# Kernel tuning notes

Hardware: AMD Instinct MI355X
Metric: run time of the kernel (lower is better)

The kernel has to match this reference:

```python
import jax, jax.numpy as jnp
import numpy as np

NEG_SLOPE = 0.2   # PyG GATConv leaky_relu default
BN_EPS = 1e-5


def setup_inputs() -> dict:
    key = jax.random.key(0)
    ks = jax.random.split(key, 6)
    B, C, N, T = 8, 128, 64, 512   # batch, in_channels, electrodes, time_steps
    H, D = 4, 32                   # heads, per-head dim; OUT = H*D = 128
    E = 256                        # knn edges (k=4 per electrode)
    OUT = H * D
    x = jax.random.normal(ks[0], (B, C, N, T), dtype=jnp.float32)
    W = jax.random.normal(ks[1], (C, H, D), dtype=jnp.float32) / np.float32(np.sqrt(C))
    att_src = jax.random.normal(ks[2], (H, D), dtype=jnp.float32) / np.float32(np.sqrt(D))
    att_dst = jax.random.normal(ks[3], (H, D), dtype=jnp.float32) / np.float32(np.sqrt(D))
    bias = jnp.zeros((OUT,), dtype=jnp.float32)
    bn_gamma = jnp.ones((OUT,), jnp.float32)
    bn_beta = jnp.zeros((OUT,), jnp.float32)
    bn_mean = jnp.zeros((OUT,), jnp.float32)   # BatchNorm running stats (eval mode)
    bn_var = jnp.ones((OUT,), jnp.float32)
    edge_index = jax.random.randint(ks[4], (2, E), 0, N, dtype=jnp.int32)
    return dict(x=x, W=W, att_src=att_src, att_dst=att_dst, bias=bias,
                bn_gamma=bn_gamma, bn_beta=bn_beta, bn_mean=bn_mean,
                bn_var=bn_var, edge_index=edge_index)


def _gat(x, W, att_src, att_dst, bias, edge_index):
    # x: [BT, N, C]; fixed graph shared across all BT slices -> fully batched
    BT, N, C = x.shape
    H, D = att_src.shape
    loops = jnp.arange(N, dtype=edge_index.dtype)
    src = jnp.concatenate([edge_index[0], loops])   # GATConv add_self_loops=True
    dst = jnp.concatenate([edge_index[1], loops])   # [E']
    h = jnp.einsum('bnc,chd->bnhd', x, W)           # [BT,N,H,D]
    a_src = jnp.einsum('bnhd,hd->bnh', h, att_src)  # [BT,N,H]
    a_dst = jnp.einsum('bnhd,hd->bnh', h, att_dst)
    scores = jax.nn.leaky_relu(a_src[:, src] + a_dst[:, dst], NEG_SLOPE)  # [BT,E',H]
    scores_e = jnp.transpose(scores, (1, 0, 2))                           # [E',BT,H]
    # segment softmax over incoming edges of each target node
    m = jax.ops.segment_max(scores_e, dst, num_segments=N)               # [N,BT,H]
    ex = jnp.exp(scores_e - m[dst])
    denom = jax.ops.segment_sum(ex, dst, num_segments=N)
    alpha = ex / denom[dst]                                               # [E',BT,H]
    msgs = alpha[..., None] * jnp.transpose(h[:, src], (1, 0, 2, 3))      # [E',BT,H,D]
    agg = jax.ops.segment_sum(msgs, dst, num_segments=N)                  # [N,BT,H,D]
    out = jnp.transpose(agg, (1, 0, 2, 3)).reshape(BT, N, H * D) + bias   # concat heads
    return out


def reference(x, W, att_src, att_dst, bias, bn_gamma, bn_beta, bn_mean, bn_var, edge_index):
    B, C, N, T = x.shape
    xt = jnp.transpose(x, (0, 3, 2, 1)).reshape(B * T, N, C)  # loop dim batched
    g = _gat(xt, W, att_src, att_dst, bias, edge_index)        # [BT,N,OUT]
    g = g.mean(axis=1)                                         # mean over nodes -> [BT,OUT]
    OUT = g.shape[-1]
    g = g.reshape(B, T, OUT).transpose(0, 2, 1)                # [B,OUT,T]
    y = (g - bn_mean[:, None]) * jax.lax.rsqrt(bn_var[:, None] + BN_EPS) \
        * bn_gamma[:, None] + bn_beta[:, None]                 # BatchNorm1d (eval)
    return y[:, :, None, :]                                    # [B,OUT,1,T]
```

## Files before the change

### kernel.cpp

```cpp
#include <hip/hip_runtime.h>
#include <math.h>

#define B_ 8
#define C_ 128
#define N_ 64
#define T_ 512
#define H_ 4
#define D_ 32
#define OUT_ 128
#define E_ 256
#define EP_ 320
#define NEG_SLOPE 0.2f
#define BN_EPS 1e-5f
#define TC 16

__global__ void setup_kernel(const float* __restrict__ W,
                             const float* __restrict__ att_src,
                             const float* __restrict__ att_dst,
                             const int* __restrict__ edge_index,
                             float* __restrict__ wa,
                             int* __restrict__ iOff_g, int* __restrict__ iSrc_g,
                             int* __restrict__ oOff_g, int* __restrict__ oDst_g) {
  __shared__ int icnt[N_], ibase[N_ + 1], ifill[N_];
  __shared__ int ocnt[N_], obase[N_ + 1], ofill[N_];
  __shared__ int esrc[EP_], edst[EP_];
  int tid = threadIdx.x;

  for (int idx = tid; idx < C_ * 8; idx += blockDim.x) {
    int c = idx >> 3, j = idx & 7, h = j & 3;
    const float* att = (j < 4) ? att_src : att_dst;
    float s = 0.f;
    for (int d = 0; d < D_; ++d)
      s += W[(c * H_ + h) * D_ + d] * att[h * D_ + d];
    wa[idx] = s;
  }
  if (tid < N_) { icnt[tid] = 0; ifill[tid] = 0; ocnt[tid] = 0; ofill[tid] = 0; }
  __syncthreads();
  for (int e = tid; e < EP_; e += blockDim.x) {
    int s, d;
    if (e < E_) { s = edge_index[e]; d = edge_index[E_ + e]; }
    else        { s = e - E_;        d = e - E_; }
    esrc[e] = s; edst[e] = d;
    atomicAdd(&icnt[d], 1);
    atomicAdd(&ocnt[s], 1);
  }
  __syncthreads();
  if (tid == 0) {
    int ai = 0, ao = 0;
    for (int n = 0; n < N_; ++n) {
      ibase[n] = ai; ai += icnt[n];
      obase[n] = ao; ao += ocnt[n];
    }
    ibase[N_] = ai; obase[N_] = ao;
  }
  __syncthreads();
  if (tid <= N_) { iOff_g[tid] = ibase[tid]; oOff_g[tid] = obase[tid]; }
  for (int e = tid; e < EP_; e += blockDim.x) {
    int s = esrc[e], d = edst[e];
    int pi = ibase[d] + atomicAdd(&ifill[d], 1);
    iSrc_g[pi] = s;
    int po = obase[s] + atomicAdd(&ofill[s], 1);
    oDst_g[po] = d;
  }
}

__global__ __launch_bounds__(256, 1)
void mega_kernel(const float* __restrict__ x,
                 const float* __restrict__ wa_g,
                 const float* __restrict__ W,
                 const int* __restrict__ iOff_g, const int* __restrict__ iSrc_g,
                 const int* __restrict__ oOff_g, const int* __restrict__ oDst_g,
                 const float* __restrict__ bias,
                 const float* __restrict__ bn_gamma,
                 const float* __restrict__ bn_beta,
                 const float* __restrict__ bn_mean,
                 const float* __restrict__ bn_var,
                 float* __restrict__ out) {
  __shared__ float a_l[8 * 64 * 20];
  __shared__ float m_l[64 * 16 * 4];
  __shared__ float inv_l[64 * 16 * 4];
  __shared__ float w_l[64 * 4 * 16];
  __shared__ float wal[C_ * 8];
  __shared__ int iOff[N_ + 1], oOff[N_ + 1];
  __shared__ int iSrc[EP_], oDst[EP_];

  const int tid = threadIdx.x;
  const int xcd = blockIdx.x & 7;
  const int jj  = blockIdx.x >> 3;
  const int pair = xcd * 16 + (jj & 15);
  const int parity = jj >> 4;
  const int b  = pair >> 4;
  const int tc = ((pair & 15) << 1) | parity;
  const int t0 = tc * TC;

  for (int i = tid; i < EP_; i += 256) { iSrc[i] = iSrc_g[i]; oDst[i] = oDst_g[i]; }
  if (tid <= N_) { iOff[tid] = iOff_g[tid]; oOff[tid] = oOff_g[tid]; }
  for (int i = tid; i < C_ * 8; i += 256) wal[i] = wa_g[i];
  __syncthreads();

  {
    const int n1 = tid >> 2, q = tid & 3;
    const float* xp = x + ((size_t)(b * C_) * N_ + n1) * T_ + t0 + q * 4;
    float acc[8][4];
#pragma unroll
    for (int j = 0; j < 8; ++j)
#pragma unroll
      for (int tt = 0; tt < 4; ++tt) acc[j][tt] = 0.f;
#pragma unroll 4
    for (int c = 0; c < C_; ++c) {
      float4 xv = *reinterpret_cast<const float4*>(xp + (size_t)c * (N_ * T_));
      float xq[4] = {xv.x, xv.y, xv.z, xv.w};
#pragma unroll
      for (int j = 0; j < 8; ++j) {
        float wj = wal[c * 8 + j];
#pragma unroll
        for (int tt = 0; tt < 4; ++tt) acc[j][tt] = fmaf(xq[tt], wj, acc[j][tt]);
      }
    }
#pragma unroll
    for (int j = 0; j < 8; ++j) {
      float4 v; v.x = acc[j][0]; v.y = acc[j][1]; v.z = acc[j][2]; v.w = acc[j][3];
      *reinterpret_cast<float4*>(&a_l[j * 1280 + n1 * 20 + q * 4]) = v;
    }
  }
  __syncthreads();

  {
    const int t = tid & 15, grp = tid >> 4;
#pragma unroll
    for (int rep = 0; rep < 4; ++rep) {
      int nd = grp + rep * 16;
      int e0 = iOff[nd], e1 = iOff[nd + 1];
      float ad0 = a_l[4 * 1280 + nd * 20 + t];
      float ad1 = a_l[5 * 1280 + nd * 20 + t];
      float ad2 = a_l[6 * 1280 + nd * 20 + t];
      float ad3 = a_l[7 * 1280 + nd * 20 + t];
      float m0 = -1e30f, m1 = -1e30f, m2 = -1e30f, m3 = -1e30f;
      for (int e = e0; e < e1; ++e) {
        int s = iSrc[e];
        float v0 = a_l[0 * 1280 + s * 20 + t] + ad0; v0 = v0 > 0.f ? v0 : NEG_SLOPE * v0;
        float v1 = a_l[1 * 1280 + s * 20 + t] + ad1; v1 = v1 > 0.f ? v1 : NEG_SLOPE * v1;
        float v2 = a_l[2 * 1280 + s * 20 + t] + ad2; v2 = v2 > 0.f ? v2 : NEG_SLOPE * v2;
        float v3 = a_l[3 * 1280 + s * 20 + t] + ad3; v3 = v3 > 0.f ? v3 : NEG_SLOPE * v3;
        m0 = fmaxf(m0, v0); m1 = fmaxf(m1, v1);
        m2 = fmaxf(m2, v2); m3 = fmaxf(m3, v3);
      }
      float d0 = 0.f, d1 = 0.f, d2 = 0.f, d3 = 0.f;
      for (int e = e0; e < e1; ++e) {
        int s = iSrc[e];
        float v0 = a_l[0 * 1280 + s * 20 + t] + ad0; v0 = v0 > 0.f ? v0 : NEG_SLOPE * v0;
        float v1 = a_l[1 * 1280 + s * 20 + t] + ad1; v1 = v1 > 0.f ? v1 : NEG_SLOPE * v1;
        float v2 = a_l[2 * 1280 + s * 20 + t] + ad2; v2 = v2 > 0.f ? v2 : NEG_SLOPE * v2;
        float v3 = a_l[3 * 1280 + s * 20 + t] + ad3; v3 = v3 > 0.f ? v3 : NEG_SLOPE * v3;
        d0 += __expf(v0 - m0); d1 += __expf(v1 - m1);
        d2 += __expf(v2 - m2); d3 += __expf(v3 - m3);
      }
      float4 mv; mv.x = m0; mv.y = m1; mv.z = m2; mv.w = m3;
      float4 iv; iv.x = 1.f / (d0 * (float)N_); iv.y = 1.f / (d1 * (float)N_);
      iv.z = 1.f / (d2 * (float)N_); iv.w = 1.f / (d3 * (float)N_);
      *reinterpret_cast<float4*>(&m_l[(nd * 16 + t) * 4]) = mv;
      *reinterpret_cast<float4*>(&inv_l[(nd * 16 + t) * 4]) = iv;
    }
  }
  __syncthreads();

  {
    const int t = tid & 15, grp = tid >> 4;
#pragma unroll
    for (int rep = 0; rep < 4; ++rep) {
      int src = grp + rep * 16;
      int e0 = oOff[src], e1 = oOff[src + 1];
      float as0 = a_l[0 * 1280 + src * 20 + t];
      float as1 = a_l[1 * 1280 + src * 20 + t];
      float as2 = a_l[2 * 1280 + src * 20 + t];
      float as3 = a_l[3 * 1280 + src * 20 + t];
      float w0 = 0.f, w1 = 0.f, w2 = 0.f, w3 = 0.f;
      for (int e = e0; e < e1; ++e) {
        int d = oDst[e];
        float4 mv = *reinterpret_cast<const float4*>(&m_l[(d * 16 + t) * 4]);
        float4 iv = *reinterpret_cast<const float4*>(&inv_l[(d * 16 + t) * 4]);
        float v0 = as0 + a_l[4 * 1280 + d * 20 + t]; v0 = v0 > 0.f ? v0 : NEG_SLOPE * v0;
        float v1 = as1 + a_l[5 * 1280 + d * 20 + t]; v1 = v1 > 0.f ? v1 : NEG_SLOPE * v1;
        float v2 = as2 + a_l[6 * 1280 + d * 20 + t]; v2 = v2 > 0.f ? v2 : NEG_SLOPE * v2;
        float v3 = as3 + a_l[7 * 1280 + d * 20 + t]; v3 = v3 > 0.f ? v3 : NEG_SLOPE * v3;
        w0 += __expf(v0 - mv.x) * iv.x;
        w1 += __expf(v1 - mv.y) * iv.y;
        w2 += __expf(v2 - mv.z) * iv.z;
        w3 += __expf(v3 - mv.w) * iv.w;
      }
      w_l[src * 64 +  0 + t] = w0;
      w_l[src * 64 + 16 + t] = w1;
      w_l[src * 64 + 32 + t] = w2;
      w_l[src * 64 + 48 + t] = w3;
    }
  }
  __syncthreads();

  {
    const int t2 = tid & 15, cl = tid >> 4;
    const float* xb = x + ((size_t)(b * C_) + cl) * N_ * T_ + t0 + t2;
    float yr[8][4];
#pragma unroll
    for (int cg = 0; cg < 8; ++cg)
#pragma unroll
      for (int h = 0; h < 4; ++h) yr[cg][h] = 0.f;
#pragma unroll 2
    for (int n = 0; n < N_; ++n) {
      float w0 = w_l[n * 64 +  0 + t2];
      float w1 = w_l[n * 64 + 16 + t2];
      float w2 = w_l[n * 64 + 32 + t2];
      float w3 = w_l[n * 64 + 48 + t2];
#pragma unroll
      for (int cg = 0; cg < 8; ++cg) {
        float xv = xb[(size_t)cg * 16 * N_ * T_ + (size_t)n * T_];
        yr[cg][0] = fmaf(xv, w0, yr[cg][0]);
        yr[cg][1] = fmaf(xv, w1, yr[cg][1]);
        yr[cg][2] = fmaf(xv, w2, yr[cg][2]);
        yr[cg][3] = fmaf(xv, w3, yr[cg][3]);
      }
    }
    float* y_l = a_l;
#pragma unroll
    for (int cg = 0; cg < 8; ++cg)
#pragma unroll
      for (int h = 0; h < 4; ++h)
        y_l[h * 2176 + (cg * 16 + cl) * 17 + t2] = yr[cg][h];
  }
  __syncthreads();

  {
    const int t3 = tid & 15, g = tid >> 4;
    const int h = g >> 2, d0 = (g & 3) * 8;
    const float* y_l = a_l;
    float acc[8];
#pragma unroll
    for (int k = 0; k < 8; ++k) acc[k] = 0.f;
#pragma unroll 4
    for (int c = 0; c < C_; ++c) {
      float yv = y_l[h * 2176 + c * 17 + t3];
      const float4 wv0 = *reinterpret_cast<const float4*>(
          &W[((size_t)c * H_ + h) * D_ + d0]);
      const float4 wv1 = *reinterpret_cast<const float4*>(
          &W[((size_t)c * H_ + h) * D_ + d0 + 4]);
      acc[0] = fmaf(yv, wv0.x, acc[0]); acc[1] = fmaf(yv, wv0.y, acc[1]);
      acc[2] = fmaf(yv, wv0.z, acc[2]); acc[3] = fmaf(yv, wv0.w, acc[3]);
      acc[4] = fmaf(yv, wv1.x, acc[4]); acc[5] = fmaf(yv, wv1.y, acc[5]);
      acc[6] = fmaf(yv, wv1.z, acc[6]); acc[7] = fmaf(yv, wv1.w, acc[7]);
    }
#pragma unroll
    for (int k = 0; k < 8; ++k) {
      int oc = h * D_ + d0 + k;
      float scale = bn_gamma[oc] * rsqrtf(bn_var[oc] + BN_EPS);
      float shift = bn_beta[oc] - bn_mean[oc] * scale;
      out[((size_t)b * OUT_ + oc) * T_ + t0 + t3] =
          (acc[k] + bias[oc]) * scale + shift;
    }
  }
}

extern "C" void kernel_launch(void* const* d_in, const int* in_sizes, int n_in,
                              void* d_out, int out_size, void* d_ws, size_t ws_size,
                              hipStream_t stream) {
  const float* x        = (const float*)d_in[0];
  const float* W        = (const float*)d_in[1];
  const float* att_src  = (const float*)d_in[2];
  const float* att_dst  = (const float*)d_in[3];
  const float* bias     = (const float*)d_in[4];
  const float* bn_gamma = (const float*)d_in[5];
  const float* bn_beta  = (const float*)d_in[6];
  const float* bn_mean  = (const float*)d_in[7];
  const float* bn_var   = (const float*)d_in[8];
  const int* edge_index = (const int*)d_in[9];
  float* out = (float*)d_out;

  char* ws = (char*)d_ws;
  float* wa   = (float*)ws;
  int* iOff_g = (int*)(ws + 4096);
  int* iSrc_g = (int*)(ws + 4608);
  int* oOff_g = (int*)(ws + 6144);
  int* oDst_g = (int*)(ws + 6656);

  setup_kernel<<<1, 256, 0, stream>>>(W, att_src, att_dst, edge_index, wa,
                                      iOff_g, iSrc_g, oOff_g, oDst_g);
  mega_kernel<<<256, 256, 0, stream>>>(x, wa, W, iOff_g, iSrc_g, oOff_g, oDst_g,
                                       bias, bn_gamma, bn_beta, bn_mean, bn_var,
                                       out);
}
```

Baseline: 77.38 us.

## Halve time chunk per block to launch 512 blocks with two blocks per CU

Reduces the per-block time tile from 16 to 8 steps, doubling the grid to 512 blocks and raising launch bounds so two blocks can co-reside per CU. Shared buffers shrink and every phase's thread mapping is redone: x loads become float2/float4 with new strides, the aggregation phase is re-tiled so each thread covers one channel and four time steps, and the XCD-aware block remap is replaced by a plain batch/chunk split. The aim is better occupancy and latency hiding for the memory-bound x reads. In exchange each block reloads the graph tables and weights for half as much work, and losing the XCD mapping may reduce L2 locality.

```diff
diff --git a/kernel.cpp b/kernel.cpp
--- a/kernel.cpp
+++ b/kernel.cpp
@@ -12,7 +12,7 @@
 #define EP_ 320
 #define NEG_SLOPE 0.2f
 #define BN_EPS 1e-5f
-#define TC 16
+#define TC 8
 
 __global__ void setup_kernel(const float* __restrict__ W,
                              const float* __restrict__ att_src,
@@ -64,7 +64,7 @@
   }
 }
 
-__global__ __launch_bounds__(256, 1)
+__global__ __launch_bounds__(256, 2)
 void mega_kernel(const float* __restrict__ x,
                  const float* __restrict__ wa_g,
                  const float* __restrict__ W,
@@ -76,22 +76,18 @@
                  const float* __restrict__ bn_mean,
                  const float* __restrict__ bn_var,
                  float* __restrict__ out) {
-  __shared__ float a_l[8 * 64 * 20];
-  __shared__ float m_l[64 * 16 * 4];
-  __shared__ float inv_l[64 * 16 * 4];
-  __shared__ float w_l[64 * 4 * 16];
+  __shared__ float a_l[8 * 64 * 12];
+  __shared__ float m_l[64 * 9 * 4];
+  __shared__ float inv_l[64 * 9 * 4];
+  __shared__ float w_l[64 * 36];
   __shared__ float wal[C_ * 8];
   __shared__ int iOff[N_ + 1], oOff[N_ + 1];
   __shared__ int iSrc[EP_], oDst[EP_];
 
   const int tid = threadIdx.x;
-  const int xcd = blockIdx.x & 7;
-  const int jj  = blockIdx.x >> 3;
-  const int pair = xcd * 16 + (jj & 15);
-  const int parity = jj >> 4;
-  const int b  = pair >> 4;
-  const int tc = ((pair & 15) << 1) | parity;
-  const int t0 = tc * TC;
+  const int b = blockIdx.x & 7;
+  const int tchunk = blockIdx.x >> 3;
+  const int t0 = tchunk * TC;
 
   for (int i = tid; i < EP_; i += 256) { iSrc[i] = iSrc_g[i]; oDst[i] = oDst_g[i]; }
   if (tid <= N_) { iOff[tid] = iOff_g[tid]; oOff[tid] = oOff_g[tid]; }
@@ -100,155 +96,146 @@
 
   {
     const int n1 = tid >> 2, q = tid & 3;
-    const float* xp = x + ((size_t)(b * C_) * N_ + n1) * T_ + t0 + q * 4;
-    float acc[8][4];
-#pragma unroll
-    for (int j = 0; j < 8; ++j)
-#pragma unroll
-      for (int tt = 0; tt < 4; ++tt) acc[j][tt] = 0.f;
-#pragma unroll 4
+    const float* xp = x + ((size_t)(b * C_) * N_ + n1) * T_ + t0 + q * 2;
+    float acc[8][2];
+#pragma unroll
+    for (int j = 0; j < 8; ++j) { acc[j][0] = 0.f; acc[j][1] = 0.f; }
+#pragma unroll 8
     for (int c = 0; c < C_; ++c) {
-      float4 xv = *reinterpret_cast<const float4*>(xp + (size_t)c * (N_ * T_));
-      float xq[4] = {xv.x, xv.y, xv.z, xv.w};
+      float2 xv = *reinterpret_cast<const float2*>(xp + (size_t)c * (N_ * T_));
 #pragma unroll
       for (int j = 0; j < 8; ++j) {
         float wj = wal[c * 8 + j];
-#pragma unroll
-        for (int tt = 0; tt < 4; ++tt) acc[j][tt] = fmaf(xq[tt], wj, acc[j][tt]);
+        acc[j][0] = fmaf(xv.x, wj, acc[j][0]);
+        acc[j][1] = fmaf(xv.y, wj, acc[j][1]);
       }
     }
 #pragma unroll
     for (int j = 0; j < 8; ++j) {
-      float4 v; v.x = acc[j][0]; v.y = acc[j][1]; v.z = acc[j][2]; v.w = acc[j][3];
-      *reinterpret_cast<float4*>(&a_l[j * 1280 + n1 * 20 + q * 4]) = v;
-    }
-  }
-  __syncthreads();
-
-  {
-    const int t = tid & 15, grp = tid >> 4;
-#pragma unroll
-    for (int rep = 0; rep < 4; ++rep) {
-      int nd = grp + rep * 16;
+      float2 v; v.x = acc[j][0]; v.y = acc[j][1];
+      *reinterpret_cast<float2*>(&a_l[j * 768 + n1 * 12 + q * 2]) = v;
+    }
+  }
+  __syncthreads();
+
+  {
+    const int t = tid & 7, grp = tid >> 3;
+#pragma unroll
+    for (int rep = 0; rep < 2; ++rep) {
+      int nd = grp + rep * 32;
       int e0 = iOff[nd], e1 = iOff[nd + 1];
-      float ad0 = a_l[4 * 1280 + nd * 20 + t];
-      float ad1 = a_l[5 * 1280 + nd * 20 + t];
-      float ad2 = a_l[6 * 1280 + nd * 20 + t];
-      float ad3 = a_l[7 * 1280 + nd * 20 + t];
+      float ad0 = a_l[4 * 768 + nd * 12 + t];
+      float ad1 = a_l[5 * 768 + nd * 12 + t];
+      float ad2 = a_l[6 * 768 + nd * 12 + t];
+      float ad3 = a_l[7 * 768 + nd * 12 + t];
       float m0 = -1e30f, m1 = -1e30f, m2 = -1e30f, m3 = -1e30f;
       for (int e = e0; e < e1; ++e) {
         int s = iSrc[e];
-        float v0 = a_l[0 * 1280 + s * 20 + t] + ad0; v0 = v0 > 0.f ? v0 : NEG_SLOPE * v0;
-        float v1 = a_l[1 * 1280 + s * 20 + t] + ad1; v1 = v1 > 0.f ? v1 : NEG_SLOPE * v1;
-        float v2 = a_l[2 * 1280 + s * 20 + t] + ad2; v2 = v2 > 0.f ? v2 : NEG_SLOPE * v2;
-        float v3 = a_l[3 * 1280 + s * 20 + t] + ad3; v3 = v3 > 0.f ? v3 : NEG_SLOPE * v3;
+        float v0 = a_l[0 * 768 + s * 12 + t] + ad0; v0 = v0 > 0.f ? v0 : NEG_SLOPE * v0;
+        float v1 = a_l[1 * 768 + s * 12 + t] + ad1; v1 = v1 > 0.f ? v1 : NEG_SLOPE * v1;
+        float v2 = a_l[2 * 768 + s * 12 + t] + ad2; v2 = v2 > 0.f ? v2 : NEG_SLOPE * v2;
+        float v3 = a_l[3 * 768 + s * 12 + t] + ad3; v3 = v3 > 0.f ? v3 : NEG_SLOPE * v3;
         m0 = fmaxf(m0, v0); m1 = fmaxf(m1, v1);
         m2 = fmaxf(m2, v2); m3 = fmaxf(m3, v3);
       }
       float d0 = 0.f, d1 = 0.f, d2 = 0.f, d3 = 0.f;
       for (int e = e0; e < e1; ++e) {
         int s = iSrc[e];
-        float v0 = a_l[0 * 1280 + s * 20 + t] + ad0; v0 = v0 > 0.f ? v0 : NEG_SLOPE * v0;
-        float v1 = a_l[1 * 1280 + s * 20 + t] + ad1; v1 = v1 > 0.f ? v1 : NEG_SLOPE * v1;
-        float v2 = a_l[2 * 1280 + s * 20 + t] + ad2; v2 = v2 > 0.f ? v2 : NEG_SLOPE * v2;
-        float v3 = a_l[3 * 1280 + s * 20 + t] + ad3; v3 = v3 > 0.f ? v3 : NEG_SLOPE * v3;
+        float v0 = a_l[0 * 768 + s * 12 + t] + ad0; v0 = v0 > 0.f ? v0 : NEG_SLOPE * v0;
+        float v1 = a_l[1 * 768 + s * 12 + t] + ad1; v1 = v1 > 0.f ? v1 : NEG_SLOPE * v1;
+        float v2 = a_l[2 * 768 + s * 12 + t] + ad2; v2 = v2 > 0.f ? v2 : NEG_SLOPE * v2;
+        float v3 = a_l[3 * 768 + s * 12 + t] + ad3; v3 = v3 > 0.f ? v3 : NEG_SLOPE * v3;
         d0 += __expf(v0 - m0); d1 += __expf(v1 - m1);
         d2 += __expf(v2 - m2); d3 += __expf(v3 - m3);
       }
       float4 mv; mv.x = m0; mv.y = m1; mv.z = m2; mv.w = m3;
       float4 iv; iv.x = 1.f / (d0 * (float)N_); iv.y = 1.f / (d1 * (float)N_);
       iv.z = 1.f / (d2 * (float)N_); iv.w = 1.f / (d3 * (float)N_);
-      *reinterpret_cast<float4*>(&m_l[(nd * 16 + t) * 4]) = mv;
-      *reinterpret_cast<float4*>(&inv_l[(nd * 16 + t) * 4]) = iv;
-    }
-  }
-  __syncthreads();
-
-  {
-    const int t = tid & 15, grp = tid >> 4;
-#pragma unroll
-    for (int rep = 0; rep < 4; ++rep) {
-      int src = grp + rep * 16;
+      *reinterpret_cast<float4*>(&m_l[(nd * 9 + t) * 4]) = mv;
+      *reinterpret_cast<float4*>(&inv_l[(nd * 9 + t) * 4]) = iv;
+    }
+  }
+  __syncthreads();
+
+  {
+    const int t = tid & 7, grp = tid >> 3;
+#pragma unroll
+    for (int rep = 0; rep < 2; ++rep) {
+      int src = grp + rep * 32;
       int e0 = oOff[src], e1 = oOff[src + 1];
-      float as0 = a_l[0 * 1280 + src * 20 + t];
-      float as1 = a_l[1 * 1280 + src * 20 + t];
-      float as2 = a_l[2 * 1280 + src * 20 + t];
-      float as3 = a_l[3 * 1280 + src * 20 + t];
+      float as0 = a_l[0 * 768 + src * 12 + t];
+      float as1 = a_l[1 * 768 + src * 12 + t];
+      float as2 = a_l[2 * 768 + src * 12 + t];
+      float as3 = a_l[3 * 768 + src * 12 + t];
       float w0 = 0.f, w1 = 0.f, w2 = 0.f, w3 = 0.f;
       for (int e = e0; e < e1; ++e) {
         int d = oDst[e];
-        float4 mv = *reinterpret_cast<const float4*>(&m_l[(d * 16 + t) * 4]);
-        float4 iv = *reinterpret_cast<const float4*>(&inv_l[(d * 16 + t) * 4]);
-        float v0 = as0 + a_l[4 * 1280 + d * 20 + t]; v0 = v0 > 0.f ? v0 : NEG_SLOPE * v0;
-        float v1 = as1 + a_l[5 * 1280 + d * 20 + t]; v1 = v1 > 0.f ? v1 : NEG_SLOPE * v1;
-        float v2 = as2 + a_l[6 * 1280 + d * 20 + t]; v2 = v2 > 0.f ? v2 : NEG_SLOPE * v2;
-        float v3 = as3 + a_l[7 * 1280 + d * 20 + t]; v3 = v3 > 0.f ? v3 : NEG_SLOPE * v3;
+        float4 mv = *reinterpret_cast<const float4*>(&m_l[(d * 9 + t) * 4]);
+        float4 iv = *reinterpret_cast<const float4*>(&inv_l[(d * 9 + t) * 4]);
+        float v0 = as0 + a_l[4 * 768 + d * 12 + t]; v0 = v0 > 0.f ? v0 : NEG_SLOPE * v0;
+        float v1 = as1 + a_l[5 * 768 + d * 12 + t]; v1 = v1 > 0.f ? v1 : NEG_SLOPE * v1;
+        float v2 = as2 + a_l[6 * 768 + d * 12 + t]; v2 = v2 > 0.f ? v2 : NEG_SLOPE * v2;
+        float v3 = as3 + a_l[7 * 768 + d * 12 + t]; v3 = v3 > 0.f ? v3 : NEG_SLOPE * v3;
         w0 += __expf(v0 - mv.x) * iv.x;
         w1 += __expf(v1 - mv.y) * iv.y;
         w2 += __expf(v2 - mv.z) * iv.z;
         w3 += __expf(v3 - mv.w) * iv.w;
       }
-      w_l[src * 64 +  0 + t] = w0;
-      w_l[src * 64 + 16 + t] = w1;
-      w_l[src * 64 + 32 + t] = w2;
-      w_l[src * 64 + 48 + t] = w3;
-    }
-  }
-  __syncthreads();
-
-  {
-    const int t2 = tid & 15, cl = tid >> 4;
-    const float* xb = x + ((size_t)(b * C_) + cl) * N_ * T_ + t0 + t2;
-    float yr[8][4];
-#pragma unroll
-    for (int cg = 0; cg < 8; ++cg)
-#pragma unroll
-      for (int h = 0; h < 4; ++h) yr[cg][h] = 0.f;
-#pragma unroll 2
+      w_l[src * 36 +  0 + t] = w0;
+      w_l[src * 36 +  8 + t] = w1;
+      w_l[src * 36 + 16 + t] = w2;
+      w_l[src * 36 + 24 + t] = w3;
+    }
+  }
+  __syncthreads();
+
+  {
+    const int cl = tid >> 1, g = tid & 1;
+    const float* xb = x + ((size_t)(b * C_) + cl) * N_ * T_ + t0 + g * 4;
+    float yr[4][4];
+#pragma unroll
+    for (int h = 0; h < 4; ++h)
+#pragma unroll
+      for (int tt = 0; tt < 4; ++tt) yr[h][tt] = 0.f;
+#pragma unroll 8
     for (int n = 0; n < N_; ++n) {
-      float w0 = w_l[n * 64 +  0 + t2];
-      float w1 = w_l[n * 64 + 16 + t2];
-      float w2 = w_l[n * 64 + 32 + t2];
-      float w3 = w_l[n * 64 + 48 + t2];
-#pragma unroll
-      for (int cg = 0; cg < 8; ++cg) {
-        float xv = xb[(size_t)cg * 16 * N_ * T_ + (size_t)n * T_];
-        yr[cg][0] = fmaf(xv, w0, yr[cg][0]);
-        yr[cg][1] = fmaf(xv, w1, yr[cg][1]);
-        yr[cg][2] = fmaf(xv, w2, yr[cg][2]);
-        yr[cg][3] = fmaf(xv, w3, yr[cg][3]);
+      float4 xv = *reinterpret_cast<const float4*>(xb + (size_t)n * T_);
+#pragma unroll
+      for (int h = 0; h < 4; ++h) {
+        float4 wv = *reinterpret_cast<const float4*>(&w_l[n * 36 + h * 8 + g * 4]);
+        yr[h][0] = fmaf(xv.x, wv.x, yr[h][0]);
+        yr[h][1] = fmaf(xv.y, wv.y, yr[h][1]);
+        yr[h][2] = fmaf(xv.z, wv.z, yr[h][2]);
+        yr[h][3] = fmaf(xv.w, wv.w, yr[h][3]);
       }
     }
     float* y_l = a_l;
 #pragma unroll
-    for (int cg = 0; cg < 8; ++cg)
-#pragma unroll
-      for (int h = 0; h < 4; ++h)
-        y_l[h * 2176 + (cg * 16 + cl) * 17 + t2] = yr[cg][h];
-  }
-  __syncthreads();
-
-  {
-    const int t3 = tid & 15, g = tid >> 4;
-    const int h = g >> 2, d0 = (g & 3) * 8;
+    for (int h = 0; h < 4; ++h) {
+      float4 v; v.x = yr[h][0]; v.y = yr[h][1]; v.z = yr[h][2]; v.w = yr[h][3];
+      y_l[h * 1152 + cl * 9 + g * 4 + 0] = v.x;
+      y_l[h * 1152 + cl * 9 + g * 4 + 1] = v.y;
+      y_l[h * 1152 + cl * 9 + g * 4 + 2] = v.z;
+      y_l[h * 1152 + cl * 9 + g * 4 + 3] = v.w;
+    }
+  }
+  __syncthreads();
+
+  {
+    const int t3 = tid & 7, g3 = tid >> 3;
+    const int h = g3 >> 3, d0 = (g3 & 7) * 4;
     const float* y_l = a_l;
-    float acc[8];
-#pragma unroll
-    for (int k = 0; k < 8; ++k) acc[k] = 0.f;
+    float acc[4] = {0.f, 0.f, 0.f, 0.f};
 #pragma unroll 4
     for (int c = 0; c < C_; ++c) {
-      float yv = y_l[h * 2176 + c * 17 + t3];
-      const float4 wv0 = *reinterpret_cast<const float4*>(
+      float yv = y_l[h * 1152 + c * 9 + t3];
+      const float4 wv = *reinterpret_cast<const float4*>(
           &W[((size_t)c * H_ + h) * D_ + d0]);
-      const float4 wv1 = *reinterpret_cast<const float4*>(
-          &W[((size_t)c * H_ + h) * D_ + d0 + 4]);
-      acc[0] = fmaf(yv, wv0.x, acc[0]); acc[1] = fmaf(yv, wv0.y, acc[1]);
-      acc[2] = fmaf(yv, wv0.z, acc[2]); acc[3] = fmaf(yv, wv0.w, acc[3]);
-      acc[4] = fmaf(yv, wv1.x, acc[4]); acc[5] = fmaf(yv, wv1.y, acc[5]);
-      acc[6] = fmaf(yv, wv1.z, acc[6]); acc[7] = fmaf(yv, wv1.w, acc[7]);
-    }
-#pragma unroll
-    for (int k = 0; k < 8; ++k) {
+      acc[0] = fmaf(yv, wv.x, acc[0]); acc[1] = fmaf(yv, wv.y, acc[1]);
+      acc[2] = fmaf(yv, wv.z, acc[2]); acc[3] = fmaf(yv, wv.w, acc[3]);
+    }
+#pragma unroll
+    for (int k = 0; k < 4; ++k) {
       int oc = h * D_ + d0 + k;
       float scale = bn_gamma[oc] * rsqrtf(bn_var[oc] + BN_EPS);
       float shift = bn_beta[oc] - bn_mean[oc] * scale;
@@ -282,7 +269,7 @@
 
   setup_kernel<<<1, 256, 0, stream>>>(W, att_src, att_dst, edge_index, wa,
                                       iOff_g, iSrc_g, oOff_g, oDst_g);
-  mega_kernel<<<256, 256, 0, stream>>>(x, wa, W, iOff_g, iSrc_g, oOff_g, oDst_g,
+  mega_kernel<<<512, 256, 0, stream>>>(x, wa, W, iOff_g, iSrc_g, oOff_g, oDst_g,
                                        bias, bn_gamma, bn_beta, bn_mean, bn_var,
                                        out);
 }
```

After: 81.77 us. 5.7% more time.

## Quadruple threads per block with split-K attention projection and LDS-staged W

Applied to the files above, without the earlier changes.

Blocks grow from 256 to 1024 threads. The attention-logit projection is split across four channel quarters and combined through a shared-memory tree reduction. Each thread now handles one node in the softmax stages and half as many channels in the aggregation. The softmax max/inverse is folded into a single scale exp(-m)/denom, and W is staged into LDS for the final projection. The goal is more memory-level parallelism and latency hiding for the x reads. The cost is extra barriers, reduction traffic and a large 112KB shared arena.

```diff
diff --git a/kernel.cpp b/kernel.cpp
--- a/kernel.cpp
+++ b/kernel.cpp
@@ -13,6 +13,7 @@
 #define NEG_SLOPE 0.2f
 #define BN_EPS 1e-5f
 #define TC 16
+#define NT_ (N_ * T_)
 
 __global__ void setup_kernel(const float* __restrict__ W,
                              const float* __restrict__ att_src,
@@ -64,10 +65,10 @@
   }
 }
 
-__global__ __launch_bounds__(256, 1)
+__global__ __launch_bounds__(1024, 1)
 void mega_kernel(const float* __restrict__ x,
                  const float* __restrict__ wa_g,
-                 const float* __restrict__ W,
+                 const float* __restrict__ Wm,
                  const int* __restrict__ iOff_g, const int* __restrict__ iSrc_g,
                  const int* __restrict__ oOff_g, const int* __restrict__ oDst_g,
                  const float* __restrict__ bias,
@@ -76,185 +77,233 @@
                  const float* __restrict__ bn_mean,
                  const float* __restrict__ bn_var,
                  float* __restrict__ out) {
-  __shared__ float a_l[8 * 64 * 20];
-  __shared__ float m_l[64 * 16 * 4];
-  __shared__ float inv_l[64 * 16 * 4];
-  __shared__ float w_l[64 * 4 * 16];
-  __shared__ float wal[C_ * 8];
-  __shared__ int iOff[N_ + 1], oOff[N_ + 1];
-  __shared__ int iSrc[EP_], oDst[EP_];
+  __shared__ __align__(16) char arena[114688];
+  float* a_l   = (float*)arena;
+  float4* redA = (float4*)(arena + 40960);
+  float4* redB = (float4*)(arena + 73728);
+  float* z_l   = (float*)(arena + 40960);
+  float* w_l   = (float*)(arena + 57344);
+  float* wstage= (float*)(arena + 40960);
+  float* wal   = (float*)(arena + 106496);
+  int* iSrc = (int*)(arena + 110592);
+  int* oDst = iSrc + EP_;
+  int* iOff = oDst + EP_;
+  int* oOff = iOff + (N_ + 1);
 
   const int tid = threadIdx.x;
-  const int xcd = blockIdx.x & 7;
-  const int jj  = blockIdx.x >> 3;
-  const int pair = xcd * 16 + (jj & 15);
-  const int parity = jj >> 4;
-  const int b  = pair >> 4;
-  const int tc = ((pair & 15) << 1) | parity;
-  const int t0 = tc * TC;
-
-  for (int i = tid; i < EP_; i += 256) { iSrc[i] = iSrc_g[i]; oDst[i] = oDst_g[i]; }
-  if (tid <= N_) { iOff[tid] = iOff_g[tid]; oOff[tid] = oOff_g[tid]; }
-  for (int i = tid; i < C_ * 8; i += 256) wal[i] = wa_g[i];
-  __syncthreads();
-
-  {
-    const int n1 = tid >> 2, q = tid & 3;
-    const float* xp = x + ((size_t)(b * C_) * N_ + n1) * T_ + t0 + q * 4;
-    float acc[8][4];
-#pragma unroll
-    for (int j = 0; j < 8; ++j)
-#pragma unroll
-      for (int tt = 0; tt < 4; ++tt) acc[j][tt] = 0.f;
-#pragma unroll 4
-    for (int c = 0; c < C_; ++c) {
-      float4 xv = *reinterpret_cast<const float4*>(xp + (size_t)c * (N_ * T_));
-      float xq[4] = {xv.x, xv.y, xv.z, xv.w};
+  const int b = blockIdx.x & 7;
+  const int tchunk = blockIdx.x >> 3;
+  const int t0 = tchunk * TC;
+
+  if (tid < EP_) { iSrc[tid] = iSrc_g[tid]; oDst[tid] = oDst_g[tid]; }
+  if (tid >= EP_ && tid < EP_ + N_ + 1) {
+    int i = tid - EP_;
+    iOff[i] = iOff_g[i]; oOff[i] = oOff_g[i];
+  }
+  if (tid < C_ * 8) wal[tid] = wa_g[tid];
+  __syncthreads();
+
+  {
+    const int q  = tid & 3;
+    const int cq = (tid >> 2) & 3;
+    const int n1 = tid >> 4;
+    const float* xp = x + ((size_t)(b * C_ + cq * 32) * N_ + n1) * T_ + t0 + q * 4;
+    float4 acc[8];
+#pragma unroll
+    for (int j = 0; j < 8; ++j) { acc[j].x = 0.f; acc[j].y = 0.f; acc[j].z = 0.f; acc[j].w = 0.f; }
+    for (int kb = 0; kb < 4; ++kb) {
+      float4 xv[8];
+#pragma unroll
+      for (int u = 0; u < 8; ++u)
+        xv[u] = *reinterpret_cast<const float4*>(xp + (size_t)(kb * 8 + u) * NT_);
+#pragma unroll
+      for (int u = 0; u < 8; ++u) {
+        const int c = cq * 32 + kb * 8 + u;
+        const float4 w0 = *reinterpret_cast<const float4*>(&wal[c * 8]);
+        const float4 w1 = *reinterpret_cast<const float4*>(&wal[c * 8 + 4]);
+        const float4 xu = xv[u];
+        acc[0].x = fmaf(xu.x, w0.x, acc[0].x); acc[0].y = fmaf(xu.y, w0.x, acc[0].y);
+        acc[0].z = fmaf(xu.z, w0.x, acc[0].z); acc[0].w = fmaf(xu.w, w0.x, acc[0].w);
+        acc[1].x = fmaf(xu.x, w0.y, acc[1].x); acc[1].y = fmaf(xu.y, w0.y, acc[1].y);
+        acc[1].z = fmaf(xu.z, w0.y, acc[1].z); acc[1].w = fmaf(xu.w, w0.y, acc[1].w);
+        acc[2].x = fmaf(xu.x, w0.z, acc[2].x); acc[2].y = fmaf(xu.y, w0.z, acc[2].y);
+        acc[2].z = fmaf(xu.z, w0.z, acc[2].z); acc[2].w = fmaf(xu.w, w0.z, acc[2].w);
+        acc[3].x = fmaf(xu.x, w0.w, acc[3].x); acc[3].y = fmaf(xu.y, w0.w, acc[3].y);
+        acc[3].z = fmaf(xu.z, w0.w, acc[3].z); acc[3].w = fmaf(xu.w, w0.w, acc[3].w);
+        acc[4].x = fmaf(xu.x, w1.x, acc[4].x); acc[4].y = fmaf(xu.y, w1.x, acc[4].y);
+        acc[4].z = fmaf(xu.z, w1.x, acc[4].z); acc[4].w = fmaf(xu.w, w1.x, acc[4].w);
+        acc[5].x = fmaf(xu.x, w1.y, acc[5].x); acc[5].y = fmaf(xu.y, w1.y, acc[5].y);
+        acc[5].z = fmaf(xu.z, w1.y, acc[5].z); acc[5].w = fmaf(xu.w, w1.y, acc[5].w);
+        acc[6].x = fmaf(xu.x, w1.z, acc[6].x); acc[6].y = fmaf(xu.y, w1.z, acc[6].y);
+        acc[6].z = fmaf(xu.z, w1.z, acc[6].z); acc[6].w = fmaf(xu.w, w1.z, acc[6].w);
+        acc[7].x = fmaf(xu.x, w1.w, acc[7].x); acc[7].y = fmaf(xu.y, w1.w, acc[7].y);
+        acc[7].z = fmaf(xu.z, w1.w, acc[7].z); acc[7].w = fmaf(xu.w, w1.w, acc[7].w);
+      }
+    }
+    if (cq == 1) {
+#pragma unroll
+      for (int j = 0; j < 8; ++j) redA[(j * 64 + n1) * 4 + q] = acc[j];
+    } else if (cq == 3) {
+#pragma unroll
+      for (int j = 0; j < 8; ++j) redB[(j * 64 + n1) * 4 + q] = acc[j];
+    }
+    __syncthreads();
+    if (cq == 0) {
 #pragma unroll
       for (int j = 0; j < 8; ++j) {
-        float wj = wal[c * 8 + j];
-#pragma unroll
-        for (int tt = 0; tt < 4; ++tt) acc[j][tt] = fmaf(xq[tt], wj, acc[j][tt]);
-      }
-    }
-#pragma unroll
-    for (int j = 0; j < 8; ++j) {
-      float4 v; v.x = acc[j][0]; v.y = acc[j][1]; v.z = acc[j][2]; v.w = acc[j][3];
-      *reinterpret_cast<float4*>(&a_l[j * 1280 + n1 * 20 + q * 4]) = v;
-    }
-  }
-  __syncthreads();
-
-  {
-    const int t = tid & 15, grp = tid >> 4;
-#pragma unroll
-    for (int rep = 0; rep < 4; ++rep) {
-      int nd = grp + rep * 16;
-      int e0 = iOff[nd], e1 = iOff[nd + 1];
-      float ad0 = a_l[4 * 1280 + nd * 20 + t];
-      float ad1 = a_l[5 * 1280 + nd * 20 + t];
-      float ad2 = a_l[6 * 1280 + nd * 20 + t];
-      float ad3 = a_l[7 * 1280 + nd * 20 + t];
-      float m0 = -1e30f, m1 = -1e30f, m2 = -1e30f, m3 = -1e30f;
-      for (int e = e0; e < e1; ++e) {
-        int s = iSrc[e];
-        float v0 = a_l[0 * 1280 + s * 20 + t] + ad0; v0 = v0 > 0.f ? v0 : NEG_SLOPE * v0;
-        float v1 = a_l[1 * 1280 + s * 20 + t] + ad1; v1 = v1 > 0.f ? v1 : NEG_SLOPE * v1;
-        float v2 = a_l[2 * 1280 + s * 20 + t] + ad2; v2 = v2 > 0.f ? v2 : NEG_SLOPE * v2;
-        float v3 = a_l[3 * 1280 + s * 20 + t] + ad3; v3 = v3 > 0.f ? v3 : NEG_SLOPE * v3;
-        m0 = fmaxf(m0, v0); m1 = fmaxf(m1, v1);
-        m2 = fmaxf(m2, v2); m3 = fmaxf(m3, v3);
-      }
-      float d0 = 0.f, d1 = 0.f, d2 = 0.f, d3 = 0.f;
-      for (int e = e0; e < e1; ++e) {
-        int s = iSrc[e];
-        float v0 = a_l[0 * 1280 + s * 20 + t] + ad0; v0 = v0 > 0.f ? v0 : NEG_SLOPE * v0;
-        float v1 = a_l[1 * 1280 + s * 20 + t] + ad1; v1 = v1 > 0.f ? v1 : NEG_SLOPE * v1;
-        float v2 = a_l[2 * 1280 + s * 20 + t] + ad2; v2 = v2 > 0.f ? v2 : NEG_SLOPE * v2;
-        float v3 = a_l[3 * 1280 + s * 20 + t] + ad3; v3 = v3 > 0.f ? v3 : NEG_SLOPE * v3;
-        d0 += __expf(v0 - m0); d1 += __expf(v1 - m1);
-        d2 += __expf(v2 - m2); d3 += __expf(v3 - m3);
-      }
-      float4 mv; mv.x = m0; mv.y = m1; mv.z = m2; mv.w = m3;
-      float4 iv; iv.x = 1.f / (d0 * (float)N_); iv.y = 1.f / (d1 * (float)N_);
-      iv.z = 1.f / (d2 * (float)N_); iv.w = 1.f / (d3 * (float)N_);
-      *reinterpret_cast<float4*>(&m_l[(nd * 16 + t) * 4]) = mv;
-      *reinterpret_cast<float4*>(&inv_l[(nd * 16 + t) * 4]) = iv;
-    }
-  }
-  __syncthreads();
-
-  {
-    const int t = tid & 15, grp = tid >> 4;
-#pragma unroll
-    for (int rep = 0; rep < 4; ++rep) {
-      int src = grp + rep * 16;
-      int e0 = oOff[src], e1 = oOff[src + 1];
-      float as0 = a_l[0 * 1280 + src * 20 + t];
-      float as1 = a_l[1 * 1280 + src * 20 + t];
-      float as2 = a_l[2 * 1280 + src * 20 + t];
-      float as3 = a_l[3 * 1280 + src * 20 + t];
-      float w0 = 0.f, w1 = 0.f, w2 = 0.f, w3 = 0.f;
-      for (int e = e0; e < e1; ++e) {
-        int d = oDst[e];
-        float4 mv = *reinterpret_cast<const float4*>(&m_l[(d * 16 + t) * 4]);
-        float4 iv = *reinterpret_cast<const float4*>(&inv_l[(d * 16 + t) * 4]);
-        float v0 = as0 + a_l[4 * 1280 + d * 20 + t]; v0 = v0 > 0.f ? v0 : NEG_SLOPE * v0;
-        float v1 = as1 + a_l[5 * 1280 + d * 20 + t]; v1 = v1 > 0.f ? v1 : NEG_SLOPE * v1;
-        float v2 = as2 + a_l[6 * 1280 + d * 20 + t]; v2 = v2 > 0.f ? v2 : NEG_SLOPE * v2;
-        float v3 = as3 + a_l[7 * 1280 + d * 20 + t]; v3 = v3 > 0.f ? v3 : NEG_SLOPE * v3;
-        w0 += __expf(v0 - mv.x) * iv.x;
-        w1 += __expf(v1 - mv.y) * iv.y;
-        w2 += __expf(v2 - mv.z) * iv.z;
-        w3 += __expf(v3 - mv.w) * iv.w;
-      }
-      w_l[src * 64 +  0 + t] = w0;
-      w_l[src * 64 + 16 + t] = w1;
-      w_l[src * 64 + 32 + t] = w2;
-      w_l[src * 64 + 48 + t] = w3;
-    }
+        float4 o = redA[(j * 64 + n1) * 4 + q];
+        acc[j].x += o.x; acc[j].y += o.y; acc[j].z += o.z; acc[j].w += o.w;
+      }
+    } else if (cq == 2) {
+#pragma unroll
+      for (int j = 0; j < 8; ++j) {
+        float4 o = redB[(j * 64 + n1) * 4 + q];
+        acc[j].x += o.x; acc[j].y += o.y; acc[j].z += o.z; acc[j].w += o.w;
+        redB[(j * 64 + n1) * 4 + q] = acc[j];
+      }
+    }
+    __syncthreads();
+    if (cq == 0) {
+#pragma unroll
+      for (int j = 0; j < 8; ++j) {
+        float4 o = redB[(j * 64 + n1) * 4 + q];
+        float4 r;
+        r.x = acc[j].x + o.x; r.y = acc[j].y + o.y;
+        r.z = acc[j].z + o.z; r.w = acc[j].w + o.w;
+        *reinterpret_cast<float4*>(&a_l[j * 1280 + n1 * 20 + q * 4]) = r;
+      }
+    }
+    __syncthreads();
+  }
+
+  {
+    const int t = tid & 15, nd = tid >> 4;
+    int e0 = iOff[nd], e1 = iOff[nd + 1];
+    float ad0 = a_l[4 * 1280 + nd * 20 + t];
+    float ad1 = a_l[5 * 1280 + nd * 20 + t];
+    float ad2 = a_l[6 * 1280 + nd * 20 + t];
+    float ad3 = a_l[7 * 1280 + nd * 20 + t];
+    float m0 = -1e30f, m1 = -1e30f, m2 = -1e30f, m3 = -1e30f;
+    for (int e = e0; e < e1; ++e) {
+      int s = iSrc[e];
+      float v0 = a_l[0 * 1280 + s * 20 + t] + ad0; v0 = v0 > 0.f ? v0 : NEG_SLOPE * v0;
+      float v1 = a_l[1 * 1280 + s * 20 + t] + ad1; v1 = v1 > 0.f ? v1 : NEG_SLOPE * v1;
+      float v2 = a_l[2 * 1280 + s * 20 + t] + ad2; v2 = v2 > 0.f ? v2 : NEG_SLOPE * v2;
+      float v3 = a_l[3 * 1280 + s * 20 + t] + ad3; v3 = v3 > 0.f ? v3 : NEG_SLOPE * v3;
+      m0 = fmaxf(m0, v0); m1 = fmaxf(m1, v1);
+      m2 = fmaxf(m2, v2); m3 = fmaxf(m3, v3);
+    }
+    float d0 = 0.f, d1 = 0.f, d2 = 0.f, d3 = 0.f;
+    for (int e = e0; e < e1; ++e) {
+      int s = iSrc[e];
+      float v0 = a_l[0 * 1280 + s * 20 + t] + ad0; v0 = v0 > 0.f ? v0 : NEG_SLOPE * v0;
+      float v1 = a_l[1 * 1280 + s * 20 + t] + ad1; v1 = v1 > 0.f ? v1 : NEG_SLOPE * v1;
+      float v2 = a_l[2 * 1280 + s * 20 + t] + ad2; v2 = v2 > 0.f ? v2 : NEG_SLOPE * v2;
+      float v3 = a_l[3 * 1280 + s * 20 + t] + ad3; v3 = v3 > 0.f ? v3 : NEG_SLOPE * v3;
+      d0 += __expf(v0 - m0); d1 += __expf(v1 - m1);
+      d2 += __expf(v2 - m2); d3 += __expf(v3 - m3);
+    }
+    float4 zv;
+    zv.x = __expf(-m0) / (d0 * (float)N_);
+    zv.y = __expf(-m1) / (d1 * (float)N_);
+    zv.z = __expf(-m2) / (d2 * (float)N_);
+    zv.w = __expf(-m3) / (d3 * (float)N_);
+    __syncthreads();
+    *reinterpret_cast<float4*>(&z_l[(nd * 16 + t) * 4]) = zv;
+  }
+  __syncthreads();
+
+  {
+    const int t = tid & 15, src = tid >> 4;
+    int e0 = oOff[src], e1 = oOff[src + 1];
+    float as0 = a_l[0 * 1280 + src * 20 + t];
+    float as1 = a_l[1 * 1280 + src * 20 + t];
+    float as2 = a_l[2 * 1280 + src * 20 + t];
+    float as3 = a_l[3 * 1280 + src * 20 + t];
+    float w0 = 0.f, w1 = 0.f, w2 = 0.f, w3 = 0.f;
+    for (int e = e0; e < e1; ++e) {
+      int d = oDst[e];
+      float4 zv = *reinterpret_cast<const float4*>(&z_l[(d * 16 + t) * 4]);
+      float v0 = as0 + a_l[4 * 1280 + d * 20 + t]; v0 = v0 > 0.f ? v0 : NEG_SLOPE * v0;
+      float v1 = as1 + a_l[5 * 1280 + d * 20 + t]; v1 = v1 > 0.f ? v1 : NEG_SLOPE * v1;
+      float v2 = as2 + a_l[6 * 1280 + d * 20 + t]; v2 = v2 > 0.f ? v2 : NEG_SLOPE * v2;
+      float v3 = as3 + a_l[7 * 1280 + d * 20 + t]; v3 = v3 > 0.f ? v3 : NEG_SLOPE * v3;
+      w0 += __expf(v0) * zv.x;
+      w1 += __expf(v1) * zv.y;
+      w2 += __expf(v2) * zv.z;
+      w3 += __expf(v3) * zv.w;
+    }
+    w_l[src * 64 +  0 + t] = w0;
+    w_l[src * 64 + 16 + t] = w1;
+    w_l[src * 64 + 32 + t] = w2;
+    w_l[src * 64 + 48 + t] = w3;
   }
   __syncthreads();
 
   {
     const int t2 = tid & 15, cl = tid >> 4;
-    const float* xb = x + ((size_t)(b * C_) + cl) * N_ * T_ + t0 + t2;
-    float yr[8][4];
-#pragma unroll
-    for (int cg = 0; cg < 8; ++cg)
-#pragma unroll
-      for (int h = 0; h < 4; ++h) yr[cg][h] = 0.f;
-#pragma unroll 2
-    for (int n = 0; n < N_; ++n) {
-      float w0 = w_l[n * 64 +  0 + t2];
-      float w1 = w_l[n * 64 + 16 + t2];
-      float w2 = w_l[n * 64 + 32 + t2];
-      float w3 = w_l[n * 64 + 48 + t2];
-#pragma unroll
-      for (int cg = 0; cg < 8; ++cg) {
-        float xv = xb[(size_t)cg * 16 * N_ * T_ + (size_t)n * T_];
-        yr[cg][0] = fmaf(xv, w0, yr[cg][0]);
-        yr[cg][1] = fmaf(xv, w1, yr[cg][1]);
-        yr[cg][2] = fmaf(xv, w2, yr[cg][2]);
-        yr[cg][3] = fmaf(xv, w3, yr[cg][3]);
+    const float* xA = x + ((size_t)(b * C_ + cl) * N_) * T_ + t0 + t2;
+    const float* xB = xA + (size_t)64 * NT_;
+    float yrA[4] = {0.f, 0.f, 0.f, 0.f};
+    float yrB[4] = {0.f, 0.f, 0.f, 0.f};
+    for (int nb = 0; nb < 8; ++nb) {
+      float xa[8], xb_[8];
+#pragma unroll
+      for (int u = 0; u < 8; ++u) {
+        xa[u]  = xA[(size_t)(nb * 8 + u) * T_];
+        xb_[u] = xB[(size_t)(nb * 8 + u) * T_];
+      }
+#pragma unroll
+      for (int u = 0; u < 8; ++u) {
+        const int n = nb * 8 + u;
+        float w0 = w_l[n * 64 +  0 + t2];
+        float w1 = w_l[n * 64 + 16 + t2];
+        float w2 = w_l[n * 64 + 32 + t2];
+        float w3 = w_l[n * 64 + 48 + t2];
+        yrA[0] = fmaf(xa[u], w0, yrA[0]); yrA[1] = fmaf(xa[u], w1, yrA[1]);
+        yrA[2] = fmaf(xa[u], w2, yrA[2]); yrA[3] = fmaf(xa[u], w3, yrA[3]);
+        yrB[0] = fmaf(xb_[u], w0, yrB[0]); yrB[1] = fmaf(xb_[u], w1, yrB[1]);
+        yrB[2] = fmaf(xb_[u], w2, yrB[2]); yrB[3] = fmaf(xb_[u], w3, yrB[3]);
       }
     }
     float* y_l = a_l;
 #pragma unroll
-    for (int cg = 0; cg < 8; ++cg)
-#pragma unroll
-      for (int h = 0; h < 4; ++h)
-        y_l[h * 2176 + (cg * 16 + cl) * 17 + t2] = yr[cg][h];
-  }
-  __syncthreads();
-
-  {
-    const int t3 = tid & 15, g = tid >> 4;
-    const int h = g >> 2, d0 = (g & 3) * 8;
+    for (int h = 0; h < 4; ++h) {
+      y_l[h * 2176 + cl * 17 + t2]        = yrA[h];
+      y_l[h * 2176 + (cl + 64) * 17 + t2] = yrB[h];
+    }
+  }
+  __syncthreads();
+
+  {
+    const float4* Wm4 = reinterpret_cast<const float4*>(Wm);
+    float4* ws4 = reinterpret_cast<float4*>(wstage);
+#pragma unroll
+    for (int r = 0; r < 4; ++r) ws4[r * 1024 + tid] = Wm4[r * 1024 + tid];
+  }
+  __syncthreads();
+  {
+    const int t3 = tid & 15;
+    const int g = tid >> 4;
+    const int h = g >> 4;
+    const int dp = g & 15;
     const float* y_l = a_l;
-    float acc[8];
-#pragma unroll
-    for (int k = 0; k < 8; ++k) acc[k] = 0.f;
-#pragma unroll 4
+    float acc0 = 0.f, acc1 = 0.f;
+#pragma unroll 8
     for (int c = 0; c < C_; ++c) {
       float yv = y_l[h * 2176 + c * 17 + t3];
-      const float4 wv0 = *reinterpret_cast<const float4*>(
-          &W[((size_t)c * H_ + h) * D_ + d0]);
-      const float4 wv1 = *reinterpret_cast<const float4*>(
-          &W[((size_t)c * H_ + h) * D_ + d0 + 4]);
-      acc[0] = fmaf(yv, wv0.x, acc[0]); acc[1] = fmaf(yv, wv0.y, acc[1]);
-      acc[2] = fmaf(yv, wv0.z, acc[2]); acc[3] = fmaf(yv, wv0.w, acc[3]);
-      acc[4] = fmaf(yv, wv1.x, acc[4]); acc[5] = fmaf(yv, wv1.y, acc[5]);
-      acc[6] = fmaf(yv, wv1.z, acc[6]); acc[7] = fmaf(yv, wv1.w, acc[7]);
-    }
-#pragma unroll
-    for (int k = 0; k < 8; ++k) {
-      int oc = h * D_ + d0 + k;
-      float scale = bn_gamma[oc] * rsqrtf(bn_var[oc] + BN_EPS);
-      float shift = bn_beta[oc] - bn_mean[oc] * scale;
-      out[((size_t)b * OUT_ + oc) * T_ + t0 + t3] =
-          (acc[k] + bias[oc]) * scale + shift;
-    }
+      const float2 wv = *reinterpret_cast<const float2*>(
+          &wstage[(c * H_ + h) * D_ + dp * 2]);
+      acc0 = fmaf(yv, wv.x, acc0);
+      acc1 = fmaf(yv, wv.y, acc1);
+    }
+    int oc = h * D_ + dp * 2;
+    float s0 = bn_gamma[oc] * rsqrtf(bn_var[oc] + BN_EPS);
+    float s1 = bn_gamma[oc + 1] * rsqrtf(bn_var[oc + 1] + BN_EPS);
+    out[((size_t)b * OUT_ + oc) * T_ + t0 + t3] =
+        (acc0 + bias[oc]) * s0 + bn_beta[oc] - bn_mean[oc] * s0;
+    out[((size_t)b * OUT_ + oc + 1) * T_ + t0 + t3] =
+        (acc1 + bias[oc + 1]) * s1 + bn_beta[oc + 1] - bn_mean[oc + 1] * s1;
   }
 }
 
@@ -282,7 +331,7 @@
 
   setup_kernel<<<1, 256, 0, stream>>>(W, att_src, att_dst, edge_index, wa,
                                       iOff_g, iSrc_g, oOff_g, oDst_g);
-  mega_kernel<<<256, 256, 0, stream>>>(x, wa, W, iOff_g, iSrc_g, oOff_g, oDst_g,
-                                       bias, bn_gamma, bn_beta, bn_mean, bn_var,
-                                       out);
+  mega_kernel<<<256, 1024, 0, stream>>>(x, wa, W, iOff_g, iSrc_g, oOff_g, oDst_g,
+                                        bias, bn_gamma, bn_beta, bn_mean, bn_var,
+                                        out);
 }
```

New measurement: 73.30 us. 5.3% less time.
